# Optimization experiments

Measured on AMD Instinct MI355X. Metric: run time of the kernel, lower is better.

## Reference

```python
import jax, jax.numpy as jnp
import numpy as np

EMBED = 1024
HEADS = 16
HEAD_DIM = EMBED // HEADS


def setup_inputs() -> dict:
    key = jax.random.key(0)
    ks = jax.random.split(key, 6)
    B, S, E = 4, 2048, EMBED
    x = jax.random.normal(ks[0], (B, S, E), dtype=jnp.float32)
    sc = 1.0 / np.sqrt(E)
    Wq = jax.random.normal(ks[1], (E, E), dtype=jnp.float32) * sc
    Wk = jax.random.normal(ks[2], (E, E), dtype=jnp.float32) * sc
    Wv = jax.random.normal(ks[3], (E, E), dtype=jnp.float32) * sc
    # Conv1d(E, E, kernel_size=3, padding=1): weight [out, in, k], bias [out]
    Wc = jax.random.normal(ks[4], (E, E, 3), dtype=jnp.float32) * (1.0 / np.sqrt(3 * E))
    bc = jax.random.normal(ks[5], (E,), dtype=jnp.float32) * 0.01
    return {"x": x, "Wq": Wq, "Wk": Wk, "Wv": Wv, "Wc": Wc, "bc": bc}


def reference(x, Wq, Wk, Wv, Wc, bc):
    B, S, E = x.shape
    H, D = HEADS, HEAD_DIM
    # nn.Linear applies x @ W.T
    Q = (x @ Wq.T).reshape(B, S, H, D).transpose(0, 2, 1, 3)  # [B,H,S,D]
    K = (x @ Wk.T).reshape(B, S, H, D).transpose(0, 2, 1, 3)
    V = (x @ Wv.T).reshape(B, S, H, D).transpose(0, 2, 1, 3)
    scores = jnp.einsum('bhqd,bhkd->bhqk', Q, K) / jnp.sqrt(jnp.float32(D))
    attn = jax.nn.softmax(scores, axis=-1)
    M = jnp.einsum('bhqk,bhkd->bhqd', attn, V)  # [B,H,S,D]
    M = M.transpose(0, 2, 1, 3).reshape(B, S, E)  # [B,S,E]
    Mc = M.transpose(0, 2, 1)  # [B,E,S] channels-first
    out = jax.lax.conv_general_dilated(
        Mc, Wc, window_strides=(1,), padding=((1, 1),),
        dimension_numbers=('NCH', 'OIH', 'NCH'))
    out = out + bc[None, :, None]
    out = out.transpose(0, 2, 1)  # [B,S,E]
    # dropout is identity at inference
    return out
```

## Files before the change

### kernel.cpp

```cpp
#include <hip/hip_runtime.h>
#include <stdint.h>

typedef __attribute__((ext_vector_type(8))) __bf16 bf16x8;
typedef __attribute__((ext_vector_type(4))) float f32x4;

#define DEVFN static __device__ __forceinline__

constexpr int Bn = 4, Sn = 2048, En = 1024, Hn = 16, Dn = 64;
constexpr int SPAD = Sn + 2;

DEVFN uint16_t f2bf(float f) {
  union { float f; uint32_t u; } a; a.f = f;
  uint32_t u = a.u;
  return (uint16_t)((u + 0x7FFFu + ((u >> 16) & 1u)) >> 16);
}

DEVFN uint32_t cvtpk(float lo, float hi) {
  uint32_t r;
  asm("v_cvt_pk_bf16_f32 %0, %1, %2" : "=v"(r) : "v"(lo), "v"(hi));
  return r;
}

DEVFN void gld16(const void* g, void* l) {
  __builtin_amdgcn_global_load_lds(
      (const __attribute__((address_space(1))) void*)(uintptr_t)(g),
      (__attribute__((address_space(3))) void*)(uint32_t)(uintptr_t)(l), 16, 0, 0);
}

DEVFN f32x4 mfma16(bf16x8 a, bf16x8 b, f32x4 c) {
  return __builtin_amdgcn_mfma_f32_16x16x32_bf16(a, b, c, 0, 0, 0);
}

__global__ void k_cvt(const float* __restrict__ src, uint16_t* __restrict__ dst, int n) {
  int idx = blockIdx.x * blockDim.x + threadIdx.x;
  int stride = gridDim.x * blockDim.x;
  for (int i = idx * 4; i < n; i += stride * 4) {
    float4 v = *reinterpret_cast<const float4*>(src + i);
    ushort4 o;
    o.x = f2bf(v.x); o.y = f2bf(v.y); o.z = f2bf(v.z); o.w = f2bf(v.w);
    *reinterpret_cast<ushort4*>(dst + i) = o;
  }
}

__global__ void k_cvt3(const float* __restrict__ a, const float* __restrict__ b,
                       const float* __restrict__ c, uint16_t* __restrict__ dst) {
  const float* s = (blockIdx.y == 0) ? a : (blockIdx.y == 1) ? b : c;
  uint16_t* d = dst + (size_t)blockIdx.y * En * En;
  int idx = blockIdx.x * blockDim.x + threadIdx.x;
  int stride = gridDim.x * blockDim.x;
  for (int i = idx * 4; i < En * En; i += stride * 4) {
    float4 v = *reinterpret_cast<const float4*>(s + i);
    ushort4 o;
    o.x = f2bf(v.x); o.y = f2bf(v.y); o.z = f2bf(v.z); o.w = f2bf(v.w);
    *reinterpret_cast<ushort4*>(d + i) = o;
  }
}

__global__ void k_pack_wc(const float* __restrict__ wc, uint16_t* __restrict__ w2,
                          uint16_t* __restrict__ mpad) {
  if (blockIdx.x >= 4096) {
    int row = blockIdx.x - 4096;
    int b = row >> 1;
    int r = (row & 1) ? (SPAD - 1) : 0;
    uint32_t* p = reinterpret_cast<uint32_t*>(mpad + (size_t)(b * SPAD + r) * En);
    for (int i = threadIdx.x; i < En / 2; i += blockDim.x) p[i] = 0u;
    return;
  }
  int idx = blockIdx.x * blockDim.x + threadIdx.x;
  int co = idx >> 10, ci = idx & 1023;
  const float* p = wc + (size_t)idx * 3;
  w2[(size_t)co * 3072 + ci]        = f2bf(p[0]);
  w2[(size_t)co * 3072 + 1024 + ci] = f2bf(p[1]);
  w2[(size_t)co * 3072 + 2048 + ci] = f2bf(p[2]);
}

__global__ __launch_bounds__(256, 2) void k_gemm_qkv(
    const uint16_t* __restrict__ xb, const uint16_t* __restrict__ wqkv,
    uint16_t* __restrict__ Q, uint16_t* __restrict__ K, uint16_t* __restrict__ VT) {
  __shared__ uint16_t As[128 * 64];
  __shared__ uint16_t Bs[128 * 64];
  const int t = threadIdx.x;
  const int lane = t & 63, w = t >> 6;
  const int wr = w >> 1, wc = w & 1;
  const int l15 = lane & 15, lg = lane >> 4;
  const int mb = blockIdx.x % 64, nb = blockIdx.x / 64;
  const int m0 = mb * 128, n0 = nb * 128;

  f32x4 acc[4][4];
#pragma unroll
  for (int i = 0; i < 4; ++i)
#pragma unroll
    for (int j = 0; j < 4; ++j) acc[i][j] = f32x4{0.f, 0.f, 0.f, 0.f};

  for (int kb = 0; kb < 1024; kb += 64) {
#pragma unroll
    for (int i = 0; i < 4; ++i) {
      int u = i * 256 + t;
      int r = u >> 3, c = u & 7;
      int cs = c ^ (r & 7);
      gld16(xb + (size_t)(m0 + r) * 1024 + kb + cs * 8, &As[(size_t)(i * 256 + w * 64) * 8]);
      gld16(wqkv + (size_t)(n0 + r) * 1024 + kb + cs * 8, &Bs[(size_t)(i * 256 + w * 64) * 8]);
    }
    __syncthreads();
#pragma unroll
    for (int kk = 0; kk < 2; ++kk) {
      bf16x8 af[4], bfr[4];
#pragma unroll
      for (int mi = 0; mi < 4; ++mi) {
        int row = wr * 64 + mi * 16 + l15;
        int g = (kk * 4 + lg) ^ (row & 7);
        af[mi] = *reinterpret_cast<const bf16x8*>(&As[row * 64 + g * 8]);
      }
#pragma unroll
      for (int ni = 0; ni < 4; ++ni) {
        int row = wc * 64 + ni * 16 + l15;
        int g = (kk * 4 + lg) ^ (row & 7);
        bfr[ni] = *reinterpret_cast<const bf16x8*>(&Bs[row * 64 + g * 8]);
      }
#pragma unroll
      for (int mi = 0; mi < 4; ++mi)
#pragma unroll
        for (int ni = 0; ni < 4; ++ni)
          acc[mi][ni] = mfma16(af[mi], bfr[ni], acc[mi][ni]);
    }
    __syncthreads();
  }
  const int which = n0 >> 10;
  if (which == 2) {
#pragma unroll
    for (int mi = 0; mi < 4; ++mi) {
#pragma unroll
      for (int ni = 0; ni < 4; ++ni) {
        int f = (n0 & 1023) + wc * 64 + ni * 16 + l15;
        int h = f >> 6, d = f & 63;
#pragma unroll
        for (int r = 0; r < 4; ++r) {
          int m = m0 + wr * 64 + mi * 16 + (lg << 2) + r;
          int b = m >> 11, s = m & 2047;
          VT[((size_t)((b * Hn + h) * Dn + d)) * Sn + s] = f2bf(acc[mi][ni][r]);
        }
      }
    }
  } else {
    uint16_t* dst = (which == 0) ? Q : K;
#pragma unroll
    for (int mi = 0; mi < 4; ++mi) {
#pragma unroll
      for (int ni = 0; ni < 4; ++ni) {
        int f = (n0 & 1023) + wc * 64 + ni * 16 + l15;
        int h = f >> 6, d = f & 63;
#pragma unroll
        for (int r = 0; r < 4; ++r) {
          int m = m0 + wr * 64 + mi * 16 + (lg << 2) + r;
          int b = m >> 11, s = m & 2047;
          dst[((size_t)((b * Hn + h) * Sn + s)) * Dn + d] = f2bf(acc[mi][ni][r]);
        }
      }
    }
  }
}

__global__ __launch_bounds__(256, 2) void k_attn(
    const uint16_t* __restrict__ Q, const uint16_t* __restrict__ K,
    const uint16_t* __restrict__ VT, uint16_t* __restrict__ mpad) {
  __shared__ __align__(16) uint16_t Ks[2][64 * 64];
  __shared__ __align__(16) uint16_t Vs[2][64 * 64];
  __shared__ __align__(16) uint16_t Pl[4][2][16 * 64];
  const int t = threadIdx.x;
  const int lane = t & 63, w = t >> 6;
  const int l15 = lane & 15, lg = lane >> 4;
  const int bh = blockIdx.x >> 3, qt = blockIdx.x & 7;
  const int q0w = qt * 256 + w * 64;

  const uint16_t* Qh = Q + (size_t)bh * Sn * Dn;
  const uint16_t* Kh = K + (size_t)bh * Sn * Dn;
  const uint16_t* Vh = VT + (size_t)bh * Dn * Sn;
  const int sw = l15 & 7;
  const float CEXP = 0.18033688011112042f;

  bf16x8 onesf;
#pragma unroll
  for (int j = 0; j < 8; ++j) onesf[j] = (__bf16)1.0f;

  const int sr = t >> 3, sc = t & 7;
  const int scs = sc ^ (sr & 7);
  const int sr2 = (256 + t) >> 3;
  const int scs2 = sc ^ (sr2 & 7);

  bf16x8 qf[4][2];
#pragma unroll
  for (int st = 0; st < 4; ++st)
#pragma unroll
    for (int kk = 0; kk < 2; ++kk)
      qf[st][kk] = *reinterpret_cast<const bf16x8*>(
          Qh + (size_t)(q0w + st * 16 + l15) * Dn + kk * 32 + lg * 8);

  f32x4 acc[4][4];
  f32x4 csum[4];
#pragma unroll
  for (int st = 0; st < 4; ++st) {
    csum[st] = f32x4{0.f, 0.f, 0.f, 0.f};
#pragma unroll
    for (int dt = 0; dt < 4; ++dt) acc[st][dt] = f32x4{0.f, 0.f, 0.f, 0.f};
  }

  gld16(Kh + (size_t)sr * Dn + scs * 8,   &Ks[0][(size_t)(w * 64) * 8]);
  gld16(Kh + (size_t)sr2 * Dn + scs2 * 8, &Ks[0][(size_t)(256 + w * 64) * 8]);
  gld16(Vh + (size_t)sr * Sn + scs * 8,   &Vs[0][(size_t)(w * 64) * 8]);
  gld16(Vh + (size_t)sr2 * Sn + scs2 * 8, &Vs[0][(size_t)(256 + w * 64) * 8]);
  __syncthreads();

  int buf = 0;
  for (int it = 0; it < Sn / 64; ++it) {
    const int kv = it * 64;
    if (it + 1 < Sn / 64) {
      const int nkv = kv + 64;
      uint16_t* kd = (uint16_t*)&Ks[buf ^ 1][0];
      uint16_t* vd = (uint16_t*)&Vs[buf ^ 1][0];
      gld16(Kh + (size_t)(nkv + sr) * Dn + scs * 8,   kd + (size_t)(w * 64) * 8);
      gld16(Kh + (size_t)(nkv + sr2) * Dn + scs2 * 8, kd + (size_t)(256 + w * 64) * 8);
      gld16(Vh + (size_t)sr * Sn + nkv + scs * 8,     vd + (size_t)(w * 64) * 8);
      gld16(Vh + (size_t)sr2 * Sn + nkv + scs2 * 8,   vd + (size_t)(256 + w * 64) * 8);
    }
    bf16x8 kf[4][2], vf[4][2];
#pragma unroll
    for (int nt = 0; nt < 4; ++nt)
#pragma unroll
      for (int kk = 0; kk < 2; ++kk) {
        int row = nt * 16 + l15;
        int g = (kk * 4 + lg) ^ (row & 7);
        kf[nt][kk] = *reinterpret_cast<const bf16x8*>(&Ks[buf][row * 64 + g * 8]);
        vf[nt][kk] = *reinterpret_cast<const bf16x8*>(&Vs[buf][row * 64 + g * 8]);
      }
#pragma unroll
    for (int st = 0; st < 4; ++st) {
      f32x4 s4[4];
#pragma unroll
      for (int nt = 0; nt < 4; ++nt) {
        f32x4 c = f32x4{0.f, 0.f, 0.f, 0.f};
#pragma unroll
        for (int kk = 0; kk < 2; ++kk) c = mfma16(kf[nt][kk], qf[st][kk], c);
        s4[nt] = c;
      }
      uint16_t* Pw = &Pl[w][st & 1][0];
#pragma unroll
      for (int nt = 0; nt < 4; ++nt) {
        float p0 = __builtin_exp2f(s4[nt][0] * CEXP);
        float p1 = __builtin_exp2f(s4[nt][1] * CEXP);
        float p2 = __builtin_exp2f(s4[nt][2] * CEXP);
        float p3 = __builtin_exp2f(s4[nt][3] * CEXP);
        uint32_t w0 = cvtpk(p0, p1);
        uint32_t w1 = cvtpk(p2, p3);
        int slot = (2 * nt + (lg >> 1)) ^ sw;
        *reinterpret_cast<uint2*>(Pw + l15 * 64 + slot * 8 + (lg & 1) * 4) = make_uint2(w0, w1);
      }
#pragma unroll
      for (int kk = 0; kk < 2; ++kk) {
        int slot = (4 * kk + lg) ^ sw;
        bf16x8 pf = *reinterpret_cast<const bf16x8*>(Pw + l15 * 64 + slot * 8);
        csum[st] = mfma16(onesf, pf, csum[st]);
#pragma unroll
        for (int dt = 0; dt < 4; ++dt)
          acc[st][dt] = mfma16(vf[dt][kk], pf, acc[st][dt]);
      }
    }
    __syncthreads();
    buf ^= 1;
  }
  const int b = bh >> 4, h = bh & 15;
#pragma unroll
  for (int st = 0; st < 4; ++st) {
    const float inv = 1.f / csum[st][0];
    uint16_t* orow = mpad + ((size_t)(b * SPAD + 1 + q0w + st * 16 + l15)) * En + h * 64;
#pragma unroll
    for (int dt = 0; dt < 4; ++dt) {
      uint32_t w0 = cvtpk(acc[st][dt][0] * inv, acc[st][dt][1] * inv);
      uint32_t w1 = cvtpk(acc[st][dt][2] * inv, acc[st][dt][3] * inv);
      *reinterpret_cast<uint2*>(orow + dt * 16 + lg * 4) = make_uint2(w0, w1);
    }
  }
}

__global__ __launch_bounds__(256, 2) void k_gemm_conv(
    const uint16_t* __restrict__ mpad, const uint16_t* __restrict__ w2,
    const float* __restrict__ bias, float* __restrict__ out) {
  __shared__ uint16_t As[128 * 64];
  __shared__ uint16_t Bs[128 * 64];
  const int t = threadIdx.x;
  const int lane = t & 63, w = t >> 6;
  const int wr = w >> 1, wc = w & 1;
  const int l15 = lane & 15, lg = lane >> 4;
  const int mb = blockIdx.x % 64, nb = blockIdx.x / 64;
  const int m0 = mb * 128, n0 = nb * 128;

  f32x4 acc[4][4];
#pragma unroll
  for (int i = 0; i < 4; ++i)
#pragma unroll
    for (int j = 0; j < 4; ++j) acc[i][j] = f32x4{0.f, 0.f, 0.f, 0.f};

  for (int kb = 0; kb < 3072; kb += 64) {
    int tap = kb >> 10;
    int cb = kb & 1023;
#pragma unroll
    for (int i = 0; i < 4; ++i) {
      int u = i * 256 + t;
      int r = u >> 3, c = u & 7;
      int cs = c ^ (r & 7);
      int m = m0 + r;
      int b = m >> 11, s = m & 2047;
      gld16(mpad + (size_t)(b * SPAD + s + tap) * 1024 + cb + cs * 8,
            &As[(size_t)(i * 256 + w * 64) * 8]);
      gld16(w2 + (size_t)(n0 + r) * 3072 + kb + cs * 8, &Bs[(size_t)(i * 256 + w * 64) * 8]);
    }
    __syncthreads();
#pragma unroll
    for (int kk = 0; kk < 2; ++kk) {
      bf16x8 af[4], bfr[4];
#pragma unroll
      for (int mi = 0; mi < 4; ++mi) {
        int row = wr * 64 + mi * 16 + l15;
        int g = (kk * 4 + lg) ^ (row & 7);
        af[mi] = *reinterpret_cast<const bf16x8*>(&As[row * 64 + g * 8]);
      }
#pragma unroll
      for (int ni = 0; ni < 4; ++ni) {
        int row = wc * 64 + ni * 16 + l15;
        int g = (kk * 4 + lg) ^ (row & 7);
        bfr[ni] = *reinterpret_cast<const bf16x8*>(&Bs[row * 64 + g * 8]);
      }
#pragma unroll
      for (int mi = 0; mi < 4; ++mi)
#pragma unroll
        for (int ni = 0; ni < 4; ++ni)
          acc[mi][ni] = mfma16(af[mi], bfr[ni], acc[mi][ni]);
    }
    __syncthreads();
  }
#pragma unroll
  for (int ni = 0; ni < 4; ++ni) {
    int co = n0 + wc * 64 + ni * 16 + l15;
    float bv = bias[co];
#pragma unroll
    for (int mi = 0; mi < 4; ++mi) {
#pragma unroll
      for (int r = 0; r < 4; ++r) {
        int m = m0 + wr * 64 + mi * 16 + (lg << 2) + r;
        out[(size_t)m * 1024 + co] = acc[mi][ni][r] + bv;
      }
    }
  }
}

extern "C" void kernel_launch(void* const* d_in, const int* in_sizes, int n_in,
                              void* d_out, int out_size, void* d_ws, size_t ws_size,
                              hipStream_t stream) {
  const float* x  = (const float*)d_in[0];
  const float* Wq = (const float*)d_in[1];
  const float* Wk = (const float*)d_in[2];
  const float* Wv = (const float*)d_in[3];
  const float* Wc = (const float*)d_in[4];
  const float* bc = (const float*)d_in[5];
  float* out = (float*)d_out;

  char* ws = (char*)d_ws;
  uint16_t* xb   = (uint16_t*)(ws);
  uint16_t* wqkv = (uint16_t*)(ws + 16777216);
  uint16_t* w2   = (uint16_t*)(ws + 23068672);
  uint16_t* Qb   = (uint16_t*)(ws + 29360128);
  uint16_t* Kb   = (uint16_t*)(ws + 46137344);
  uint16_t* VTb  = (uint16_t*)(ws + 62914560);
  uint16_t* mpad = (uint16_t*)(ws + 96468992);

  k_cvt<<<2048, 256, 0, stream>>>(x, xb, Bn * Sn * En);
  k_cvt3<<<dim3(256, 3), 256, 0, stream>>>(Wq, Wk, Wv, wqkv);
  k_pack_wc<<<4104, 256, 0, stream>>>(Wc, w2, mpad);
  k_gemm_qkv<<<24 * 64, 256, 0, stream>>>(xb, wqkv, Qb, Kb, VTb);
  k_attn<<<512, 256, 0, stream>>>(Qb, Kb, VTb, mpad);
  k_gemm_conv<<<8 * 64, 256, 0, stream>>>(mpad, w2, bc, out);
}
```

Measured before the change: 342.0 us.

## Double-buffer GEMM tiles with vmcnt waits, fold softmax scale into Q, remap attention blocks

Both GEMM kernels get double-buffered LDS tiles. The next K-slab is prefetched with global_load_lds while the current one is consumed, and explicit vmcnt waits plus raw s_barrier replace __syncthreads, so load latency overlaps MFMA work. The attention kernel uses the same waitcnt/barrier scheme. The exp2 scale constant is folded into Q in the QKV GEMM epilogue, which removes a multiply per score. Attention blocks are also remapped so that consecutive block IDs span different heads. Doubling LDS per GEMM block (64KB) may reduce occupancy, and the hand-coded vmcnt counts must match the number of outstanding loads.

```diff
diff --git a/kernel.cpp b/kernel.cpp
--- a/kernel.cpp
+++ b/kernel.cpp
@@ -8,6 +8,7 @@
 
 constexpr int Bn = 4, Sn = 2048, En = 1024, Hn = 16, Dn = 64;
 constexpr int SPAD = Sn + 2;
+constexpr float CEXP = 0.18033688011112042f;
 
 DEVFN uint16_t f2bf(float f) {
   union { float f; uint32_t u; } a; a.f = f;
@@ -29,6 +30,21 @@
 
 DEVFN f32x4 mfma16(bf16x8 a, bf16x8 b, f32x4 c) {
   return __builtin_amdgcn_mfma_f32_16x16x32_bf16(a, b, c, 0, 0, 0);
+}
+
+template <int N> DEVFN void waitcnt_vm() {
+  if constexpr (N == 0)  asm volatile("s_waitcnt vmcnt(0)" ::: "memory");
+  else if constexpr (N == 4) asm volatile("s_waitcnt vmcnt(4)" ::: "memory");
+  else                   asm volatile("s_waitcnt vmcnt(8)" ::: "memory");
+}
+DEVFN void barrier_pre() {
+  __builtin_amdgcn_sched_barrier(0);
+  __builtin_amdgcn_s_barrier();
+  __builtin_amdgcn_sched_barrier(0);
+}
+DEVFN void barrier_post() {
+  __builtin_amdgcn_sched_barrier(0);
+  __builtin_amdgcn_s_barrier();
 }
 
 __global__ void k_cvt(const float* __restrict__ src, uint16_t* __restrict__ dst, int n) {
@@ -77,8 +93,8 @@
 __global__ __launch_bounds__(256, 2) void k_gemm_qkv(
     const uint16_t* __restrict__ xb, const uint16_t* __restrict__ wqkv,
     uint16_t* __restrict__ Q, uint16_t* __restrict__ K, uint16_t* __restrict__ VT) {
-  __shared__ uint16_t As[128 * 64];
-  __shared__ uint16_t Bs[128 * 64];
+  __shared__ __align__(16) uint16_t As[2][128 * 64];
+  __shared__ __align__(16) uint16_t Bs[2][128 * 64];
   const int t = threadIdx.x;
   const int lane = t & 63, w = t >> 6;
   const int wr = w >> 1, wc = w & 1;
@@ -92,16 +108,25 @@
 #pragma unroll
     for (int j = 0; j < 4; ++j) acc[i][j] = f32x4{0.f, 0.f, 0.f, 0.f};
 
-  for (int kb = 0; kb < 1024; kb += 64) {
+  auto stage = [&](int kb, int bsel) {
 #pragma unroll
     for (int i = 0; i < 4; ++i) {
       int u = i * 256 + t;
       int r = u >> 3, c = u & 7;
       int cs = c ^ (r & 7);
-      gld16(xb + (size_t)(m0 + r) * 1024 + kb + cs * 8, &As[(size_t)(i * 256 + w * 64) * 8]);
-      gld16(wqkv + (size_t)(n0 + r) * 1024 + kb + cs * 8, &Bs[(size_t)(i * 256 + w * 64) * 8]);
-    }
-    __syncthreads();
+      gld16(xb + (size_t)(m0 + r) * 1024 + kb + cs * 8, &As[bsel][(size_t)(i * 256 + w * 64) * 8]);
+      gld16(wqkv + (size_t)(n0 + r) * 1024 + kb + cs * 8, &Bs[bsel][(size_t)(i * 256 + w * 64) * 8]);
+    }
+  };
+
+  stage(0, 0);
+  int buf = 0;
+  for (int it = 0; it < 16; ++it) {
+    if (it + 1 < 16) { stage((it + 1) * 64, buf ^ 1); waitcnt_vm<8>(); }
+    else waitcnt_vm<0>();
+    barrier_pre();
+    const uint16_t* Ab = &As[buf][0];
+    const uint16_t* Bb = &Bs[buf][0];
 #pragma unroll
     for (int kk = 0; kk < 2; ++kk) {
       bf16x8 af[4], bfr[4];
@@ -109,13 +134,13 @@
       for (int mi = 0; mi < 4; ++mi) {
         int row = wr * 64 + mi * 16 + l15;
         int g = (kk * 4 + lg) ^ (row & 7);
-        af[mi] = *reinterpret_cast<const bf16x8*>(&As[row * 64 + g * 8]);
+        af[mi] = *reinterpret_cast<const bf16x8*>(&Ab[row * 64 + g * 8]);
       }
 #pragma unroll
       for (int ni = 0; ni < 4; ++ni) {
         int row = wc * 64 + ni * 16 + l15;
         int g = (kk * 4 + lg) ^ (row & 7);
-        bfr[ni] = *reinterpret_cast<const bf16x8*>(&Bs[row * 64 + g * 8]);
+        bfr[ni] = *reinterpret_cast<const bf16x8*>(&Bb[row * 64 + g * 8]);
       }
 #pragma unroll
       for (int mi = 0; mi < 4; ++mi)
@@ -123,9 +148,16 @@
         for (int ni = 0; ni < 4; ++ni)
           acc[mi][ni] = mfma16(af[mi], bfr[ni], acc[mi][ni]);
     }
-    __syncthreads();
+    barrier_post();
+    buf ^= 1;
   }
   const int which = n0 >> 10;
+  if (which == 0) {
+#pragma unroll
+    for (int mi = 0; mi < 4; ++mi)
+#pragma unroll
+      for (int ni = 0; ni < 4; ++ni) acc[mi][ni] *= CEXP;
+  }
   if (which == 2) {
 #pragma unroll
     for (int mi = 0; mi < 4; ++mi) {
@@ -169,14 +201,14 @@
   const int t = threadIdx.x;
   const int lane = t & 63, w = t >> 6;
   const int l15 = lane & 15, lg = lane >> 4;
-  const int bh = blockIdx.x >> 3, qt = blockIdx.x & 7;
+  const int bh = (blockIdx.x & 7) * 8 + ((blockIdx.x >> 3) & 7);
+  const int qt = blockIdx.x >> 6;
   const int q0w = qt * 256 + w * 64;
 
   const uint16_t* Qh = Q + (size_t)bh * Sn * Dn;
   const uint16_t* Kh = K + (size_t)bh * Sn * Dn;
   const uint16_t* Vh = VT + (size_t)bh * Dn * Sn;
   const int sw = l15 & 7;
-  const float CEXP = 0.18033688011112042f;
 
   bf16x8 onesf;
 #pragma unroll
@@ -187,6 +219,15 @@
   const int sr2 = (256 + t) >> 3;
   const int scs2 = sc ^ (sr2 & 7);
 
+  auto stageKV = [&](int kv, int bsel) {
+    uint16_t* kd = (uint16_t*)&Ks[bsel][0];
+    uint16_t* vd = (uint16_t*)&Vs[bsel][0];
+    gld16(Kh + (size_t)(kv + sr) * Dn + scs * 8,   kd + (size_t)(w * 64) * 8);
+    gld16(Kh + (size_t)(kv + sr2) * Dn + scs2 * 8, kd + (size_t)(256 + w * 64) * 8);
+    gld16(Vh + (size_t)sr * Sn + kv + scs * 8,     vd + (size_t)(w * 64) * 8);
+    gld16(Vh + (size_t)sr2 * Sn + kv + scs2 * 8,   vd + (size_t)(256 + w * 64) * 8);
+  };
+
   bf16x8 qf[4][2];
 #pragma unroll
   for (int st = 0; st < 4; ++st)
@@ -204,24 +245,15 @@
     for (int dt = 0; dt < 4; ++dt) acc[st][dt] = f32x4{0.f, 0.f, 0.f, 0.f};
   }
 
-  gld16(Kh + (size_t)sr * Dn + scs * 8,   &Ks[0][(size_t)(w * 64) * 8]);
-  gld16(Kh + (size_t)sr2 * Dn + scs2 * 8, &Ks[0][(size_t)(256 + w * 64) * 8]);
-  gld16(Vh + (size_t)sr * Sn + scs * 8,   &Vs[0][(size_t)(w * 64) * 8]);
-  gld16(Vh + (size_t)sr2 * Sn + scs2 * 8, &Vs[0][(size_t)(256 + w * 64) * 8]);
-  __syncthreads();
-
+  stageKV(0, 0);
   int buf = 0;
-  for (int it = 0; it < Sn / 64; ++it) {
-    const int kv = it * 64;
-    if (it + 1 < Sn / 64) {
-      const int nkv = kv + 64;
-      uint16_t* kd = (uint16_t*)&Ks[buf ^ 1][0];
-      uint16_t* vd = (uint16_t*)&Vs[buf ^ 1][0];
-      gld16(Kh + (size_t)(nkv + sr) * Dn + scs * 8,   kd + (size_t)(w * 64) * 8);
-      gld16(Kh + (size_t)(nkv + sr2) * Dn + scs2 * 8, kd + (size_t)(256 + w * 64) * 8);
-      gld16(Vh + (size_t)sr * Sn + nkv + scs * 8,     vd + (size_t)(w * 64) * 8);
-      gld16(Vh + (size_t)sr2 * Sn + nkv + scs2 * 8,   vd + (size_t)(256 + w * 64) * 8);
-    }
+  constexpr int NT = Sn / 64;
+  for (int it = 0; it < NT; ++it) {
+    if (it + 1 < NT) { stageKV((it + 1) * 64, buf ^ 1); waitcnt_vm<4>(); }
+    else waitcnt_vm<0>();
+    barrier_pre();
+    const uint16_t* Kb = &Ks[buf][0];
+    const uint16_t* Vb = &Vs[buf][0];
     bf16x8 kf[4][2], vf[4][2];
 #pragma unroll
     for (int nt = 0; nt < 4; ++nt)
@@ -229,8 +261,8 @@
       for (int kk = 0; kk < 2; ++kk) {
         int row = nt * 16 + l15;
         int g = (kk * 4 + lg) ^ (row & 7);
-        kf[nt][kk] = *reinterpret_cast<const bf16x8*>(&Ks[buf][row * 64 + g * 8]);
-        vf[nt][kk] = *reinterpret_cast<const bf16x8*>(&Vs[buf][row * 64 + g * 8]);
+        kf[nt][kk] = *reinterpret_cast<const bf16x8*>(&Kb[row * 64 + g * 8]);
+        vf[nt][kk] = *reinterpret_cast<const bf16x8*>(&Vb[row * 64 + g * 8]);
       }
 #pragma unroll
     for (int st = 0; st < 4; ++st) {
@@ -245,10 +277,10 @@
       uint16_t* Pw = &Pl[w][st & 1][0];
 #pragma unroll
       for (int nt = 0; nt < 4; ++nt) {
-        float p0 = __builtin_exp2f(s4[nt][0] * CEXP);
-        float p1 = __builtin_exp2f(s4[nt][1] * CEXP);
-        float p2 = __builtin_exp2f(s4[nt][2] * CEXP);
-        float p3 = __builtin_exp2f(s4[nt][3] * CEXP);
+        float p0 = __builtin_exp2f(s4[nt][0]);
+        float p1 = __builtin_exp2f(s4[nt][1]);
+        float p2 = __builtin_exp2f(s4[nt][2]);
+        float p3 = __builtin_exp2f(s4[nt][3]);
         uint32_t w0 = cvtpk(p0, p1);
         uint32_t w1 = cvtpk(p2, p3);
         int slot = (2 * nt + (lg >> 1)) ^ sw;
@@ -264,7 +296,7 @@
           acc[st][dt] = mfma16(vf[dt][kk], pf, acc[st][dt]);
       }
     }
-    __syncthreads();
+    barrier_post();
     buf ^= 1;
   }
   const int b = bh >> 4, h = bh & 15;
@@ -284,8 +316,8 @@
 __global__ __launch_bounds__(256, 2) void k_gemm_conv(
     const uint16_t* __restrict__ mpad, const uint16_t* __restrict__ w2,
     const float* __restrict__ bias, float* __restrict__ out) {
-  __shared__ uint16_t As[128 * 64];
-  __shared__ uint16_t Bs[128 * 64];
+  __shared__ __align__(16) uint16_t As[2][128 * 64];
+  __shared__ __align__(16) uint16_t Bs[2][128 * 64];
   const int t = threadIdx.x;
   const int lane = t & 63, w = t >> 6;
   const int wr = w >> 1, wc = w & 1;
@@ -299,7 +331,7 @@
 #pragma unroll
     for (int j = 0; j < 4; ++j) acc[i][j] = f32x4{0.f, 0.f, 0.f, 0.f};
 
-  for (int kb = 0; kb < 3072; kb += 64) {
+  auto stage = [&](int kb, int bsel) {
     int tap = kb >> 10;
     int cb = kb & 1023;
 #pragma unroll
@@ -310,10 +342,19 @@
       int m = m0 + r;
       int b = m >> 11, s = m & 2047;
       gld16(mpad + (size_t)(b * SPAD + s + tap) * 1024 + cb + cs * 8,
-            &As[(size_t)(i * 256 + w * 64) * 8]);
-      gld16(w2 + (size_t)(n0 + r) * 3072 + kb + cs * 8, &Bs[(size_t)(i * 256 + w * 64) * 8]);
-    }
-    __syncthreads();
+            &As[bsel][(size_t)(i * 256 + w * 64) * 8]);
+      gld16(w2 + (size_t)(n0 + r) * 3072 + kb + cs * 8, &Bs[bsel][(size_t)(i * 256 + w * 64) * 8]);
+    }
+  };
+
+  stage(0, 0);
+  int buf = 0;
+  for (int it = 0; it < 48; ++it) {
+    if (it + 1 < 48) { stage((it + 1) * 64, buf ^ 1); waitcnt_vm<8>(); }
+    else waitcnt_vm<0>();
+    barrier_pre();
+    const uint16_t* Ab = &As[buf][0];
+    const uint16_t* Bb = &Bs[buf][0];
 #pragma unroll
     for (int kk = 0; kk < 2; ++kk) {
       bf16x8 af[4], bfr[4];
@@ -321,13 +362,13 @@
       for (int mi = 0; mi < 4; ++mi) {
         int row = wr * 64 + mi * 16 + l15;
         int g = (kk * 4 + lg) ^ (row & 7);
-        af[mi] = *reinterpret_cast<const bf16x8*>(&As[row * 64 + g * 8]);
+        af[mi] = *reinterpret_cast<const bf16x8*>(&Ab[row * 64 + g * 8]);
       }
 #pragma unroll
       for (int ni = 0; ni < 4; ++ni) {
         int row = wc * 64 + ni * 16 + l15;
         int g = (kk * 4 + lg) ^ (row & 7);
-        bfr[ni] = *reinterpret_cast<const bf16x8*>(&Bs[row * 64 + g * 8]);
+        bfr[ni] = *reinterpret_cast<const bf16x8*>(&Bb[row * 64 + g * 8]);
       }
 #pragma unroll
       for (int mi = 0; mi < 4; ++mi)
@@ -335,7 +376,8 @@
         for (int ni = 0; ni < 4; ++ni)
           acc[mi][ni] = mfma16(af[mi], bfr[ni], acc[mi][ni]);
     }
-    __syncthreads();
+    barrier_post();
+    buf ^= 1;
   }
 #pragma unroll
   for (int ni = 0; ni < 4; ++ni) {
```

New measurement: 325.6 us. 4.8% less time.
